# Kernel tuning notes

Hardware: AMD Instinct MI355X
Metric: run time of the kernel (lower is better)

The kernel has to match this reference:

```python
import jax, jax.numpy as jnp
import numpy as np

LAMBDA_ENTROPY = 0.1
LAMBDA_REPULSION = 0.5
LAMBDA_INTER = 0.3
TEMPERATURE = 1.0
EPS = 1e-8


def setup_inputs() -> dict:
    key = jax.random.key(0)
    k1, k2 = jax.random.split(key)
    membership = jax.random.uniform(k1, (16384, 64, 32), dtype=jnp.float32)   # (N,F,K) soft bin assignments
    teacher_preds = jax.random.uniform(k2, (16384, 128), dtype=jnp.float32)   # (N,C)
    return {"membership": membership, "teacher_preds": teacher_preds}


def reference(membership, teacher_preds):
    N, F, K = membership.shape
    # --- weighted centroids per (feature, bin) ---
    bin_mass = membership.sum(axis=0) + EPS                       # (F,K)
    sum_weighted_y = jnp.einsum('nfk,nc->fkc', membership, teacher_preds)  # avoids (N,F,K,C)
    centroids = sum_weighted_y / bin_mass[..., None]              # (F,K,C)
    # --- weighted intra-bin variance: ||y_n - c_fk||^2 expanded, no (N,F,K,C) tensor ---
    y_sq = jnp.sum(teacher_preds * teacher_preds, axis=-1)        # (N,)
    c_sq = jnp.sum(centroids * centroids, axis=-1)                # (F,K)
    cross = jnp.einsum('nc,fkc->nfk', teacher_preds, centroids)   # (N,F,K)
    dist_sq = y_sq[:, None, None] + c_sq[None, :, :] - 2.0 * cross
    weighted_variance = jnp.sum(membership * dist_sq, axis=0) / bin_mass  # (F,K)
    loss_dispersion = weighted_variance.sum()
    # --- bin-occupancy entropy ---
    p_bins = bin_mass / N                                         # (F,K)
    loss_entropy = jnp.sum(p_bins * jnp.log(p_bins + EPS))
    # --- neighbor repulsion between adjacent bin centroids ---
    neighbor_dist = jnp.sum((centroids[:, :-1, :] - centroids[:, 1:, :]) ** 2, axis=-1)  # (F,K-1)
    loss_repulsion = jnp.sum(jnp.exp(-neighbor_dist / TEMPERATURE))
    # --- all-pairs inter-bin dispersion, batched over F (replaces python loop) ---
    dots = jnp.einsum('fkc,fjc->fkj', centroids, centroids)       # (F,K,K)
    pairwise = c_sq[:, :, None] + c_sq[:, None, :] - 2.0 * dots
    triu = jnp.triu(jnp.ones((K, K), dtype=centroids.dtype), k=1)  # strictly upper
    loss_inter = jnp.sum(jnp.exp(-pairwise / TEMPERATURE) * triu) / F
    total = (loss_dispersion
             + LAMBDA_ENTROPY * loss_entropy
             + LAMBDA_REPULSION * loss_repulsion
             + LAMBDA_INTER * loss_inter)
    return total, loss_dispersion, loss_entropy, loss_repulsion, loss_inter
```

## Files before the change

### kernel.cpp

```cpp
#include <hip/hip_runtime.h>
#include <math.h>

#define N_PTS   16384
#define F_DIM   64
#define K_BINS  32
#define C_DIM   128
#define FK      2048
#define CP      144
#define CW      132
#define EPS_F   1e-8f

typedef _Float16 f16x8 __attribute__((ext_vector_type(8)));
typedef float    f32x4 __attribute__((ext_vector_type(4)));

static __device__ inline unsigned pack_h2(float a, float b) {
    union { _Float16 h[2]; unsigned u; } x;
    x.h[0] = (_Float16)a; x.h[1] = (_Float16)b;
    return x.u;
}

__global__ __launch_bounds__(256) void build_yt_k(const float* __restrict__ Y,
                                                  _Float16* __restrict__ Yt) {
    __shared__ __align__(16) float Yl[64][132];
    __shared__ float ysql[64];
    const int t  = threadIdx.x;
    const int n0 = blockIdx.x * 64;
    const int nl = t >> 5;
    const int c4 = t & 31;
#pragma unroll
    for (int p = 0; p < 8; ++p) {
        const int n = p * 8 + nl;
        const float4 v = reinterpret_cast<const float4*>(Y + (size_t)(n0 + n) * C_DIM)[c4];
        reinterpret_cast<float4*>(Yl[n])[c4] = v;
        float sq = v.x * v.x + v.y * v.y + v.z * v.z + v.w * v.w;
#pragma unroll
        for (int m = 16; m >= 1; m >>= 1) sq += __shfl_xor(sq, m, 64);
        if (c4 == 0) ysql[n] = sq;
    }
    __syncthreads();
    unsigned* YtU = (unsigned*)Yt;
    const int nd0 = n0 >> 1;
    const int n2  = t & 31;
    const int rr  = t >> 5;
#pragma unroll
    for (int p = 0; p < 16; ++p) {
        const int c = p * 8 + rr;
        YtU[(size_t)c * (N_PTS / 2) + nd0 + n2] = pack_h2(Yl[2 * n2][c], Yl[2 * n2 + 1][c]);
    }
    if (t < 32) {
        YtU[(size_t)128 * (N_PTS / 2) + nd0 + t] = pack_h2(ysql[2 * t], ysql[2 * t + 1]);
    } else if (t < 64) {
        YtU[(size_t)129 * (N_PTS / 2) + nd0 + (t - 32)] = 0x3C003C00u;
    }
    for (int idx = t; idx < 14 * 32; idx += 256) {
        YtU[(size_t)(130 + (idx >> 5)) * (N_PTS / 2) + nd0 + (idx & 31)] = 0u;
    }
}

__global__ __launch_bounds__(256) void gemm_k(const float* __restrict__ M,
                                              const _Float16* __restrict__ Yt,
                                              float* __restrict__ wpart,
                                              int cn) {
    const int t    = threadIdx.x;
    const int fk0  = blockIdx.x * 128;
    const int ch   = blockIdx.y;
    const int n0   = ch * cn;
    const int w    = t >> 6;
    const int l    = t & 63;
    const int quad = l >> 4;
    const int cl   = l & 15;
    const int fkA  = fk0 + w * 32 + cl;

    f32x4 acc[2][9] = {};

    for (int nb = 0; nb < cn; nb += 32) {
        const int nbase = n0 + nb + quad * 8;
        f16x8 b[9];
#pragma unroll
        for (int ct = 0; ct < 9; ++ct)
            b[ct] = *reinterpret_cast<const f16x8*>(
                Yt + (size_t)(ct * 16 + cl) * N_PTS + nbase);
        f16x8 a0, a1;
#pragma unroll
        for (int j = 0; j < 8; ++j) {
            const float* row = M + (size_t)(nbase + j) * FK;
            a0[j] = (_Float16)row[fkA];
            a1[j] = (_Float16)row[fkA + 16];
        }
#pragma unroll
        for (int ct = 0; ct < 9; ++ct) {
            acc[0][ct] = __builtin_amdgcn_mfma_f32_16x16x32_f16(a0, b[ct], acc[0][ct], 0, 0, 0);
            acc[1][ct] = __builtin_amdgcn_mfma_f32_16x16x32_f16(a1, b[ct], acc[1][ct], 0, 0, 0);
        }
    }

    float* wp = wpart + (size_t)ch * FK * CW;
#pragma unroll
    for (int mt = 0; mt < 2; ++mt) {
#pragma unroll
        for (int ct = 0; ct < 9; ++ct) {
            const int c = ct * 16 + cl;
            if (c < CW) {
#pragma unroll
                for (int r = 0; r < 4; ++r) {
                    const int fk = fk0 + w * 32 + mt * 16 + quad * 4 + r;
                    wp[(size_t)fk * CW + c] = acc[mt][ct][r];
                }
            }
        }
    }
}

__global__ __launch_bounds__(128) void reduce_w_k(const float* __restrict__ wpart,
                                                  float* __restrict__ W, int nchunk) {
    const int idx = blockIdx.x * 128 + threadIdx.x;
    const float4* src = reinterpret_cast<const float4*>(wpart);
    const size_t cs = (size_t)FK * CW / 4;
    float4 s0 = make_float4(0.f, 0.f, 0.f, 0.f), s1 = s0, s2 = s0, s3 = s0;
    int ch = 0;
    for (; ch + 3 < nchunk; ch += 4) {
        const float4 a = src[idx + (size_t)(ch + 0) * cs];
        const float4 b = src[idx + (size_t)(ch + 1) * cs];
        const float4 c = src[idx + (size_t)(ch + 2) * cs];
        const float4 d = src[idx + (size_t)(ch + 3) * cs];
        s0.x += a.x; s0.y += a.y; s0.z += a.z; s0.w += a.w;
        s1.x += b.x; s1.y += b.y; s1.z += b.z; s1.w += b.w;
        s2.x += c.x; s2.y += c.y; s2.z += c.z; s2.w += c.w;
        s3.x += d.x; s3.y += d.y; s3.z += d.z; s3.w += d.w;
    }
    for (; ch < nchunk; ++ch) {
        const float4 a = src[idx + (size_t)ch * cs];
        s0.x += a.x; s0.y += a.y; s0.z += a.z; s0.w += a.w;
    }
    float4 r;
    r.x = (s0.x + s1.x) + (s2.x + s3.x);
    r.y = (s0.y + s1.y) + (s2.y + s3.y);
    r.z = (s0.z + s1.z) + (s2.z + s3.z);
    r.w = (s0.w + s1.w) + (s2.w + s3.w);
    reinterpret_cast<float4*>(W)[idx] = r;
}

__global__ __launch_bounds__(256) void epilogue_k(const float* __restrict__ W,
                                                  float* __restrict__ fpart) {
    __shared__ __align__(16) float Wl[32][CW];
    __shared__ float Bv[32], Binv[32], S1v[32], csq[32];
    __shared__ float scr[32][8];
    __shared__ float4 red4[256];
    const int t = threadIdx.x;
    const int f = blockIdx.x;

    for (int e = t; e < 32 * 33; e += 256) {
        const int k = e / 33, c4 = e % 33;
        reinterpret_cast<float4*>(Wl[k])[c4] =
            reinterpret_cast<const float4*>(W + (size_t)(f * 32 + k) * CW)[c4];
    }
    __syncthreads();
    if (t < 32) {
        const float B = Wl[t][129] + EPS_F;
        Bv[t] = B; Binv[t] = 1.0f / B; S1v[t] = Wl[t][128];
    }
    __syncthreads();
    {
        const int k = t >> 3, g = t & 7;
        const float ib = Binv[k];
        float s = 0.f;
        for (int c = g * 16; c < g * 16 + 16; ++c) {
            const float v = Wl[k][c] * ib;
            Wl[k][c] = v;
            s = fmaf(v, v, s);
        }
        scr[k][g] = s;
    }
    __syncthreads();
    if (t < 32) {
        float s = 0.f;
#pragma unroll
        for (int g = 0; g < 8; ++g) s += scr[t][g];
        csq[t] = s;
    }
    __syncthreads();

    float my_disp = 0.f, my_ent = 0.f, my_rep = 0.f, my_inter = 0.f;
    if (t < 32) {
        my_disp = (S1v[t] - csq[t] * (Bv[t] + EPS_F)) * Binv[t];
        const float p = Bv[t] * (1.0f / (float)N_PTS);
        my_ent = p * logf(p + EPS_F);
    }
    {
        const int pr = t >> 3, g = t & 7;
        float s = 0.f;
        if (pr < 31) {
            for (int c = g * 16; c < g * 16 + 16; ++c) {
                const float d = Wl[pr][c] - Wl[pr + 1][c];
                s = fmaf(d, d, s);
            }
        }
        __syncthreads();
        scr[pr][g] = s;
    }
    __syncthreads();
    if (t < 31) {
        float d = 0.f;
#pragma unroll
        for (int g = 0; g < 8; ++g) d += scr[t][g];
        my_rep = expf(-d);
    }
#pragma unroll
    for (int s4 = 0; s4 < 4; ++s4) {
        const int slot = t + s4 * 256;
        const int k = slot >> 5, j = slot & 31;
        if (k < j) {
            float dot = 0.f;
            for (int c4 = 0; c4 < 32; ++c4) {
                const float4 a = reinterpret_cast<const float4*>(Wl[k])[c4];
                const float4 b = reinterpret_cast<const float4*>(Wl[j])[c4];
                dot = fmaf(a.x, b.x, dot); dot = fmaf(a.y, b.y, dot);
                dot = fmaf(a.z, b.z, dot); dot = fmaf(a.w, b.w, dot);
            }
            my_inter += expf(-(csq[k] + csq[j] - 2.0f * dot));
        }
    }
    red4[t] = make_float4(my_disp, my_ent, my_rep, my_inter);
    __syncthreads();
    for (int off = 128; off >= 1; off >>= 1) {
        if (t < off) {
            const float4 a = red4[t], b = red4[t + off];
            red4[t] = make_float4(a.x + b.x, a.y + b.y, a.z + b.z, a.w + b.w);
        }
        __syncthreads();
    }
    if (t == 0) {
        fpart[f * 4 + 0] = red4[0].x;
        fpart[f * 4 + 1] = red4[0].y;
        fpart[f * 4 + 2] = red4[0].z;
        fpart[f * 4 + 3] = red4[0].w;
    }
}

__global__ void final_reduce_k(const float* __restrict__ fpart,
                               float* __restrict__ out) {
    const int t = threadIdx.x;
    float4 v = reinterpret_cast<const float4*>(fpart)[t];
#pragma unroll
    for (int m = 32; m >= 1; m >>= 1) {
        v.x += __shfl_xor(v.x, m, 64);
        v.y += __shfl_xor(v.y, m, 64);
        v.z += __shfl_xor(v.z, m, 64);
        v.w += __shfl_xor(v.w, m, 64);
    }
    if (t == 0) {
        const float disp  = v.x, ent = v.y, rep = v.z;
        const float inter = v.w * (1.0f / (float)F_DIM);
        out[0] = disp + 0.1f * ent + 0.5f * rep + 0.3f * inter;
        out[1] = disp;
        out[2] = ent;
        out[3] = rep;
        out[4] = inter;
    }
}

extern "C" void kernel_launch(void* const* d_in, const int* in_sizes, int n_in,
                              void* d_out, int out_size, void* d_ws, size_t ws_size,
                              hipStream_t stream) {
    const float* M = (const float*)d_in[0];
    const float* Y = (const float*)d_in[1];
    float* out = (float*)d_out;
    char*  ws  = (char*)d_ws;

    const size_t ytBytes = (size_t)CP * N_PTS * sizeof(_Float16);
    const size_t wBytes  = (size_t)FK * CW * sizeof(float);

    _Float16* Yt    = (_Float16*)ws;
    float*    W     = (float*)(ws + ytBytes);
    float*    fpart = (float*)(ws + ytBytes + wBytes);
    float*    wpart = (float*)(ws + ytBytes + wBytes + 1024);

    const size_t used = ytBytes + wBytes + 1024;
    int nchunk = 32;
    while (nchunk > 1 && used + (size_t)nchunk * wBytes > ws_size) nchunk >>= 1;
    const int cn = N_PTS / nchunk;

    build_yt_k<<<dim3(N_PTS / 64), dim3(256), 0, stream>>>(Y, Yt);
    gemm_k<<<dim3(16, nchunk), dim3(256), 0, stream>>>(M, Yt, wpart, cn);
    reduce_w_k<<<dim3(FK * CW / 4 / 128), dim3(128), 0, stream>>>(wpart, W, nchunk);
    epilogue_k<<<dim3(F_DIM), dim3(256), 0, stream>>>(W, fpart);
    final_reduce_k<<<dim3(1), dim3(64), 0, stream>>>(fpart, out);
}
```

Baseline: 241.3 us.

## Software-pipeline gemm_k loads with double-buffered registers and halve FK tile

After: 270.0 us. 11.9% more time.

```diff
diff --git a/kernel.cpp b/kernel.cpp
--- a/kernel.cpp
+++ b/kernel.cpp
@@ -62,50 +62,74 @@
                                               float* __restrict__ wpart,
                                               int cn) {
     const int t    = threadIdx.x;
-    const int fk0  = blockIdx.x * 128;
+    const int fk0  = blockIdx.x * 64;
     const int ch   = blockIdx.y;
     const int n0   = ch * cn;
     const int w    = t >> 6;
     const int l    = t & 63;
     const int quad = l >> 4;
     const int cl   = l & 15;
-    const int fkA  = fk0 + w * 32 + cl;
-
-    f32x4 acc[2][9] = {};
-
-    for (int nb = 0; nb < cn; nb += 32) {
-        const int nbase = n0 + nb + quad * 8;
-        f16x8 b[9];
+    const int fkA  = fk0 + w * 16 + cl;
+    const _Float16* yt = Yt + (size_t)cl * N_PTS;
+    const float*    mp = M + fkA;
+
+    f32x4 acc[9] = {};
+    f16x8 b0[9], b1[9];
+    float a0r[8], a1r[8];
+
+    int nbase = n0 + quad * 8;
+#pragma unroll
+    for (int ct = 0; ct < 9; ++ct)
+        b0[ct] = *reinterpret_cast<const f16x8*>(yt + (size_t)(ct * 16) * N_PTS + nbase);
+#pragma unroll
+    for (int j = 0; j < 8; ++j)
+        a0r[j] = mp[(size_t)(nbase + j) * FK];
+
+    for (int nb = 0; nb < cn; nb += 64) {
+        const int nb1 = nbase + 32;
 #pragma unroll
         for (int ct = 0; ct < 9; ++ct)
-            b[ct] = *reinterpret_cast<const f16x8*>(
-                Yt + (size_t)(ct * 16 + cl) * N_PTS + nbase);
-        f16x8 a0, a1;
-#pragma unroll
-        for (int j = 0; j < 8; ++j) {
-            const float* row = M + (size_t)(nbase + j) * FK;
-            a0[j] = (_Float16)row[fkA];
-            a1[j] = (_Float16)row[fkA + 16];
-        }
-#pragma unroll
-        for (int ct = 0; ct < 9; ++ct) {
-            acc[0][ct] = __builtin_amdgcn_mfma_f32_16x16x32_f16(a0, b[ct], acc[0][ct], 0, 0, 0);
-            acc[1][ct] = __builtin_amdgcn_mfma_f32_16x16x32_f16(a1, b[ct], acc[1][ct], 0, 0, 0);
-        }
+            b1[ct] = *reinterpret_cast<const f16x8*>(yt + (size_t)(ct * 16) * N_PTS + nb1);
+#pragma unroll
+        for (int j = 0; j < 8; ++j)
+            a1r[j] = mp[(size_t)(nb1 + j) * FK];
+        {
+            f16x8 a;
+#pragma unroll
+            for (int j = 0; j < 8; ++j) a[j] = (_Float16)a0r[j];
+#pragma unroll
+            for (int ct = 0; ct < 9; ++ct)
+                acc[ct] = __builtin_amdgcn_mfma_f32_16x16x32_f16(a, b0[ct], acc[ct], 0, 0, 0);
+        }
+        const int nb2 = nbase + 64;
+        if (nb + 64 < cn) {
+#pragma unroll
+            for (int ct = 0; ct < 9; ++ct)
+                b0[ct] = *reinterpret_cast<const f16x8*>(yt + (size_t)(ct * 16) * N_PTS + nb2);
+#pragma unroll
+            for (int j = 0; j < 8; ++j)
+                a0r[j] = mp[(size_t)(nb2 + j) * FK];
+        }
+        {
+            f16x8 a;
+#pragma unroll
+            for (int j = 0; j < 8; ++j) a[j] = (_Float16)a1r[j];
+#pragma unroll
+            for (int ct = 0; ct < 9; ++ct)
+                acc[ct] = __builtin_amdgcn_mfma_f32_16x16x32_f16(a, b1[ct], acc[ct], 0, 0, 0);
+        }
+        nbase = nb2;
     }
 
     float* wp = wpart + (size_t)ch * FK * CW;
 #pragma unroll
-    for (int mt = 0; mt < 2; ++mt) {
-#pragma unroll
-        for (int ct = 0; ct < 9; ++ct) {
-            const int c = ct * 16 + cl;
-            if (c < CW) {
-#pragma unroll
-                for (int r = 0; r < 4; ++r) {
-                    const int fk = fk0 + w * 32 + mt * 16 + quad * 4 + r;
-                    wp[(size_t)fk * CW + c] = acc[mt][ct][r];
-                }
+    for (int ct = 0; ct < 9; ++ct) {
+        const int c = ct * 16 + cl;
+        if (c < CW) {
+#pragma unroll
+            for (int r = 0; r < 4; ++r) {
+                const int fk = fk0 + w * 16 + quad * 4 + r;
+                wp[(size_t)fk * CW + c] = acc[ct][r];
             }
         }
     }
@@ -281,7 +305,7 @@
     const int cn = N_PTS / nchunk;
 
     build_yt_k<<<dim3(N_PTS / 64), dim3(256), 0, stream>>>(Y, Yt);
-    gemm_k<<<dim3(16, nchunk), dim3(256), 0, stream>>>(M, Yt, wpart, cn);
+    gemm_k<<<dim3(32, nchunk), dim3(256), 0, stream>>>(M, Yt, wpart, cn);
     reduce_w_k<<<dim3(FK * CW / 4 / 128), dim3(128), 0, stream>>>(wpart, W, nchunk);
     epilogue_k<<<dim3(F_DIM), dim3(256), 0, stream>>>(W, fpart);
     final_reduce_k<<<dim3(1), dim3(64), 0, stream>>>(fpart, out);
```
